# Kernel optimization log

Measured on AMD Instinct MI355X. Metric: run time of the kernel, lower is better.

The kernel has to match this reference:

```python
import jax, jax.numpy as jnp
import numpy as np

BANDWIDTH = 1.0  # init arg `bandwidth`
N, V, C = 8, 2048, 64


def setup_inputs() -> dict:
    key = jax.random.key(0)
    k1, k2 = jax.random.split(key)
    x = jax.random.normal(k1, (N, V, C), dtype=jnp.float32)
    # nn.Parameter(torch.rand(V, V)) -> uniform[0,1)
    weight = jax.random.uniform(k2, (V, V), dtype=jnp.float32)
    return {"x": x, "weight": weight}


def _pairwise_l2(x):
    # x: (N, V, C) -> dist[n,i,j] = ||x[n,i] - x[n,j]||_2, without the O(V^2*C) blow-up
    sq = jnp.sum(x * x, axis=-1)                                  # (N, V)
    d2 = sq[:, :, None] + sq[:, None, :] - 2.0 * jnp.einsum('nic,njc->nij', x, x)
    d2 = jnp.maximum(d2, 0.0)
    # safe sqrt: subgradient 0 at 0 (matches torch.norm), avoids NaN grads on the diagonal
    safe = jnp.where(d2 > 0, d2, 1.0)
    return jnp.where(d2 > 0, jnp.sqrt(safe), 0.0)


def reference(x, weight):
    dist = _pairwise_l2(x)                                        # (N, V, V)
    adj = jnp.exp((-0.5 / (BANDWIDTH ** 2)) * dist)               # Gaussian kernel on L2 (not squared)
    adj = jnp.einsum('nij,jk->nik', adj, weight)                  # (N, V, V) @ (V, V)
    return jax.nn.softmax(adj, axis=-1)
```

## Files before the change

kernel.cpp:

```cpp
#include <hip/hip_runtime.h>
#include <hip/hip_bf16.h>
#include <hip/hip_fp16.h>
#include <math.h>

#define V 2048
#define C 64
#define NB 8
#define M_TOTAL (NB * V)

typedef __attribute__((ext_vector_type(8))) short bf16x8;
typedef __attribute__((ext_vector_type(4))) float f32x4;

static __device__ __forceinline__ unsigned short f2bf(float f) {
    __hip_bfloat16 h = __float2bfloat16(f);
    return *reinterpret_cast<unsigned short*>(&h);
}
static __device__ __forceinline__ unsigned short f2h(float f) {
    __half h = __float2half(f);
    return *reinterpret_cast<unsigned short*>(&h);
}
static __device__ __forceinline__ float h2f(unsigned short u) {
    __half h = *reinterpret_cast<__half*>(&u);
    return __half2float(h);
}

#define GLOAD_LDS16(g, l)                                                        \
    __builtin_amdgcn_global_load_lds((const __attribute__((address_space(1))) void*)(g), \
                                     (__attribute__((address_space(3))) void*)(l), 16, 0, 0)


__global__ __launch_bounds__(256) void q_kernel(const float* __restrict__ x,
                                                float* __restrict__ q) {
    const int gw   = blockIdx.x * 4 + (threadIdx.x >> 6);
    const int lane = threadIdx.x & 63;
    const int lr = lane & 15, lq = lane >> 4;

    const float* rp = x + (size_t)(gw * 16 + lr) * C + lq * 8;
    float4 f0 = *(const float4*)(rp);
    float4 f1 = *(const float4*)(rp + 4);
    float4 f2 = *(const float4*)(rp + 32);
    float4 f3 = *(const float4*)(rp + 36);

    bf16x8 a0, a1;
    a0[0] = (short)f2bf(f0.x); a0[1] = (short)f2bf(f0.y);
    a0[2] = (short)f2bf(f0.z); a0[3] = (short)f2bf(f0.w);
    a0[4] = (short)f2bf(f1.x); a0[5] = (short)f2bf(f1.y);
    a0[6] = (short)f2bf(f1.z); a0[7] = (short)f2bf(f1.w);
    a1[0] = (short)f2bf(f2.x); a1[1] = (short)f2bf(f2.y);
    a1[2] = (short)f2bf(f2.z); a1[3] = (short)f2bf(f2.w);
    a1[4] = (short)f2bf(f3.x); a1[5] = (short)f2bf(f3.y);
    a1[6] = (short)f2bf(f3.z); a1[7] = (short)f2bf(f3.w);

    f32x4 acc = (f32x4){0.f, 0.f, 0.f, 0.f};
    acc = __builtin_amdgcn_mfma_f32_16x16x32_bf16(a0, a0, acc, 0, 0, 0);
    acc = __builtin_amdgcn_mfma_f32_16x16x32_bf16(a1, a1, acc, 0, 0, 0);

    const int r = lr;
    if (lq == (r >> 2)) q[gw * 16 + r] = acc[r & 3];
}

__global__ __launch_bounds__(256) void adj_mfma(const float* __restrict__ x,
                                                const float* __restrict__ q,
                                                unsigned short* __restrict__ adjb) {
    const int n  = blockIdx.z;
    const int i0 = blockIdx.y * 128;
    const int j0 = blockIdx.x * 128;
    const size_t nV = (size_t)n * V;

    __shared__ short Xi[128][72];
    __shared__ short Xj[128][72];
    __shared__ float Qi[128];
    __shared__ float Qj[128];

    const float* xn = x + nV * C;
    const int tid = threadIdx.x;

    for (int idx = tid; idx < 1024; idx += 256) {
        const int row = idx >> 3;
        const int c8  = (idx & 7) * 8;
        float4 ai0 = *(const float4*)(xn + (size_t)(i0 + row) * C + c8);
        float4 ai1 = *(const float4*)(xn + (size_t)(i0 + row) * C + c8 + 4);
        float4 aj0 = *(const float4*)(xn + (size_t)(j0 + row) * C + c8);
        float4 aj1 = *(const float4*)(xn + (size_t)(j0 + row) * C + c8 + 4);
        bf16x8 pi, pj;
        pi[0] = (short)f2bf(ai0.x); pi[1] = (short)f2bf(ai0.y);
        pi[2] = (short)f2bf(ai0.z); pi[3] = (short)f2bf(ai0.w);
        pi[4] = (short)f2bf(ai1.x); pi[5] = (short)f2bf(ai1.y);
        pi[6] = (short)f2bf(ai1.z); pi[7] = (short)f2bf(ai1.w);
        pj[0] = (short)f2bf(aj0.x); pj[1] = (short)f2bf(aj0.y);
        pj[2] = (short)f2bf(aj0.z); pj[3] = (short)f2bf(aj0.w);
        pj[4] = (short)f2bf(aj1.x); pj[5] = (short)f2bf(aj1.y);
        pj[6] = (short)f2bf(aj1.z); pj[7] = (short)f2bf(aj1.w);
        *(bf16x8*)&Xi[row][c8] = pi;
        *(bf16x8*)&Xj[row][c8] = pj;
    }
    if (tid < 128)       Qi[tid]        = q[nV + i0 + tid];
    else                 Qj[tid - 128]  = q[nV + j0 + (tid - 128)];
    __syncthreads();

    const int wid  = tid >> 6;
    const int lane = tid & 63;
    const int wr = wid >> 1, wc = wid & 1;
    const int lr = lane & 15, lq = lane >> 4;

    bf16x8 a[4][2], b[4][2];
#pragma unroll
    for (int m = 0; m < 4; ++m) {
        a[m][0] = *(const bf16x8*)&Xi[wr * 64 + m * 16 + lr][lq * 8];
        a[m][1] = *(const bf16x8*)&Xi[wr * 64 + m * 16 + lr][32 + lq * 8];
    }
#pragma unroll
    for (int nn = 0; nn < 4; ++nn) {
        b[nn][0] = *(const bf16x8*)&Xj[wc * 64 + nn * 16 + lr][lq * 8];
        b[nn][1] = *(const bf16x8*)&Xj[wc * 64 + nn * 16 + lr][32 + lq * 8];
    }

#pragma unroll
    for (int m = 0; m < 4; ++m) {
#pragma unroll
        for (int nn = 0; nn < 4; ++nn) {
            f32x4 g = (f32x4){0.f, 0.f, 0.f, 0.f};
            g = __builtin_amdgcn_mfma_f32_16x16x32_bf16(a[m][0], b[nn][0], g, 0, 0, 0);
            g = __builtin_amdgcn_mfma_f32_16x16x32_bf16(a[m][1], b[nn][1], g, 0, 0, 0);
            const int col_l = wc * 64 + nn * 16 + lr;
            const float qj = Qj[col_l];
#pragma unroll
            for (int r = 0; r < 4; ++r) {
                const int row_l = wr * 64 + m * 16 + lq * 4 + r;
                float d2 = Qi[row_l] + qj - 2.0f * g[r];
                d2 = fmaxf(d2, 0.0f);
                const float e = expf(-0.5f * sqrtf(d2));
                adjb[(nV + i0 + row_l) * V + j0 + col_l] = f2bf(e);
            }
        }
    }
}

__global__ __launch_bounds__(256) void wt_kernel(const float* __restrict__ w,
                                                 unsigned short* __restrict__ wt) {
    __shared__ float tile[64][65];
    const int r0 = blockIdx.y * 64, c0 = blockIdx.x * 64;
    const int tr = threadIdx.x >> 4;
    const int tc4 = (threadIdx.x & 15) << 2;
#pragma unroll
    for (int it = 0; it < 4; ++it) {
        const int r = tr + 16 * it;
        float4 v = *(const float4*)(w + (size_t)(r0 + r) * V + c0 + tc4);
        tile[r][tc4 + 0] = v.x; tile[r][tc4 + 1] = v.y;
        tile[r][tc4 + 2] = v.z; tile[r][tc4 + 3] = v.w;
    }
    __syncthreads();
#pragma unroll
    for (int it = 0; it < 4; ++it) {
        const int cr = tr + 16 * it;
        ushort4 o;
        o.x = f2bf(tile[tc4 + 0][cr]);
        o.y = f2bf(tile[tc4 + 1][cr]);
        o.z = f2bf(tile[tc4 + 2][cr]);
        o.w = f2bf(tile[tc4 + 3][cr]);
        *(ushort4*)(wt + (size_t)(c0 + cr) * V + r0 + tc4) = o;
    }
}

__device__ __forceinline__ void stage_region(char* smem, int regionOff,
                                             const unsigned short* gbase,
                                             int tile, int ks, int tid) {
#pragma unroll
    for (int s = 0; s < 2; ++s) {
        const int off = s * 8192 + tid * 16;
        const int row = off >> 6;
        const int pb  = off & 63;
        const int lb  = pb ^ (((row >> 1) & 3) << 4);
        const unsigned short* g = gbase + (size_t)row * V + tile * 64 + ks * 32 + (lb >> 1);
        GLOAD_LDS16(g, smem + regionOff + off);
    }
}

#define LDS_FRAG(BUF, BOFF, KS, ROW)                                             \
    (*(const bf16x8*)(smem + (BUF) * 65536 + (BOFF) + (KS) * 16384 +             \
                      (ROW) * 64 + (lqb ^ ((((ROW) >> 1) & 3) << 4))))

#define PHASE(BUF, MS, KS, LOADB, STAGE_STMT, WAITV)                             \
    {                                                                            \
        bf16x8 af[4];                                                            \
        _Pragma("unroll") for (int m = 0; m < 4; ++m) {                          \
            const int row = wr128 + ((MS) + m) * 16 + lr;                        \
            af[m] = LDS_FRAG(BUF, 0, KS, row);                                   \
        }                                                                        \
        if (LOADB) {                                                             \
            _Pragma("unroll") for (int n = 0; n < 4; ++n) {                      \
                const int row = wc64 + n * 16 + lr;                              \
                bf[n] = LDS_FRAG(BUF, 32768, KS, row);                           \
            }                                                                    \
        }                                                                        \
        STAGE_STMT;                                                              \
        if (WAITV) {                                                             \
            asm volatile("s_waitcnt vmcnt(6)" ::: "memory");                     \
            __builtin_amdgcn_sched_barrier(0);                                   \
        }                                                                        \
        __builtin_amdgcn_s_barrier();                                            \
        asm volatile("s_waitcnt lgkmcnt(0)" ::: "memory");                       \
        __builtin_amdgcn_sched_barrier(0);                                       \
        __builtin_amdgcn_s_setprio(1);                                           \
        _Pragma("unroll") for (int m = 0; m < 4; ++m)                            \
            _Pragma("unroll") for (int n = 0; n < 4; ++n)                        \
                acc[(MS) + m][n] = __builtin_amdgcn_mfma_f32_16x16x32_bf16(      \
                    af[m], bf[n], acc[(MS) + m][n], 0, 0, 0);                    \
        __builtin_amdgcn_s_setprio(0);                                           \
        __builtin_amdgcn_s_barrier();                                            \
    }

template <int FUSED>
__global__ __launch_bounds__(512, 2) void gemm_8ph(const unsigned short* __restrict__ adjb,
                                                   const unsigned short* __restrict__ wtb,
                                                   float* __restrict__ out,
                                                   unsigned short* __restrict__ expw,
                                                   float* __restrict__ partial) {
    extern __shared__ char smem[];

    const int bid = blockIdx.x;
    const int swz = (bid & 7) * 64 + (bid >> 3);
    const int by = swz >> 3;
    const int bx = swz & 7;
    const int i0 = by * 256;
    const int n0 = bx * 256;

    const int tid  = threadIdx.x;
    const int wid  = tid >> 6;
    const int lane = tid & 63;
    const int wr = wid >> 2, wc = wid & 3;
    const int wr128 = wr * 128, wc64 = wc * 64;
    const int lr = lane & 15, lq = lane >> 4;
    const int lqb = lq * 16;

    const unsigned short* gA = adjb + (size_t)i0 * V;
    const unsigned short* gB = wtb  + (size_t)n0 * V;

    f32x4 acc[8][4];
#pragma unroll
    for (int m = 0; m < 8; ++m)
#pragma unroll
        for (int n = 0; n < 4; ++n) acc[m][n] = (f32x4){0.f, 0.f, 0.f, 0.f};

    stage_region(smem, 32768,         gB, 0, 0, tid);
    stage_region(smem, 0,             gA, 0, 0, tid);
    stage_region(smem, 49152,         gB, 0, 1, tid);
    stage_region(smem, 16384,         gA, 0, 1, tid);
    stage_region(smem, 65536 + 32768, gB, 1, 0, tid);
    stage_region(smem, 65536 + 0,     gA, 1, 0, tid);
    stage_region(smem, 65536 + 49152, gB, 1, 1, tid);
    asm volatile("s_waitcnt vmcnt(6)" ::: "memory");
    __builtin_amdgcn_sched_barrier(0);
    __builtin_amdgcn_s_barrier();

    bf16x8 bf[4];

#pragma unroll 1
    for (int i = 0; i < 16; ++i) {
        const int t1b = 2 * i + 1;
        const int t2  = (2 * i + 2 < 32) ? 2 * i + 2 : 31;
        const int t3  = (2 * i + 3 < 32) ? 2 * i + 3 : 31;

        PHASE(0, 0, 0, true,  stage_region(smem, 65536 + 16384, gA, t1b, 1, tid), false)
        PHASE(0, 4, 0, false, stage_region(smem, 32768,         gB, t2,  0, tid), false)
        PHASE(0, 0, 1, true,  stage_region(smem, 0,             gA, t2,  0, tid), false)
        PHASE(0, 4, 1, false, stage_region(smem, 49152,         gB, t2,  1, tid), true)
        PHASE(1, 0, 0, true,  stage_region(smem, 16384,         gA, t2,  1, tid), false)
        PHASE(1, 4, 0, false, stage_region(smem, 65536 + 32768, gB, t3,  0, tid), false)
        PHASE(1, 0, 1, true,  stage_region(smem, 65536 + 0,     gA, t3,  0, tid), false)
        PHASE(1, 4, 1, false, stage_region(smem, 65536 + 49152, gB, t3,  1, tid), true)
    }

    if (FUSED) {
        unsigned short* ep = expw + (size_t)(i0 + wr128) * V + n0 + wc64;
        const int slot = bx * 4 + wc;
#pragma unroll
        for (int m = 0; m < 8; ++m) {
            float rp[4] = {0.f, 0.f, 0.f, 0.f};
#pragma unroll
            for (int n = 0; n < 4; ++n)
#pragma unroll
                for (int r = 0; r < 4; ++r) {
                    const float e = expf(acc[m][n][r]);
                    rp[r] += e;
                    ep[(size_t)(m * 16 + lq * 4 + r) * V + n * 16 + lr] = f2h(e);
                }
#pragma unroll
            for (int r = 0; r < 4; ++r) {
                rp[r] += __shfl_xor(rp[r], 1);
                rp[r] += __shfl_xor(rp[r], 2);
                rp[r] += __shfl_xor(rp[r], 4);
                rp[r] += __shfl_xor(rp[r], 8);
            }
            if (lr == 0) {
#pragma unroll
                for (int r = 0; r < 4; ++r)
                    partial[(size_t)(i0 + wr128 + m * 16 + lq * 4 + r) * 32 + slot] = rp[r];
            }
        }
    } else {
        float* op = out + (size_t)(i0 + wr128) * V + n0 + wc64;
#pragma unroll
        for (int m = 0; m < 8; ++m)
#pragma unroll
            for (int n = 0; n < 4; ++n)
#pragma unroll
                for (int r = 0; r < 4; ++r)
                    op[(size_t)(m * 16 + lq * 4 + r) * V + n * 16 + lr] = acc[m][n][r];
    }
}

__global__ __launch_bounds__(256) void normalize_kernel(const unsigned short* __restrict__ expw,
                                                        const float* __restrict__ partial,
                                                        float* __restrict__ out) {
    const int row  = blockIdx.x * 4 + (threadIdx.x >> 6);
    const int lane = threadIdx.x & 63;

    float s = (lane < 32) ? partial[(size_t)row * 32 + lane] : 0.0f;
#pragma unroll
    for (int o = 32; o; o >>= 1) s += __shfl_xor(s, o);
    const float inv = 1.0f / s;

    const unsigned short* ip = expw + (size_t)row * V;
    float* op = out + (size_t)row * V;
#pragma unroll
    for (int t = 0; t < 4; ++t) {
        const int base = (t * 64 + lane) * 8;
        ushort4 u0 = *(const ushort4*)(ip + base);
        ushort4 u1 = *(const ushort4*)(ip + base + 4);
        float4 o0, o1;
        o0.x = h2f(u0.x) * inv; o0.y = h2f(u0.y) * inv;
        o0.z = h2f(u0.z) * inv; o0.w = h2f(u0.w) * inv;
        o1.x = h2f(u1.x) * inv; o1.y = h2f(u1.y) * inv;
        o1.z = h2f(u1.z) * inv; o1.w = h2f(u1.w) * inv;
        *(float4*)(op + base)     = o0;
        *(float4*)(op + base + 4) = o1;
    }
}

__global__ __launch_bounds__(256) void gemm_mfma(const unsigned short* __restrict__ adjb,
                                                 const unsigned short* __restrict__ wtb,
                                                 float* __restrict__ out) {
    const int bid = blockIdx.x;
    const int swz = (bid & 7) * 256 + (bid >> 3);
    const int by = swz >> 4;
    const int bx = swz & 15;
    const int i0 = by * 128;
    const int n0 = bx * 128;

    __shared__ alignas(16) unsigned short As[128 * 32];
    __shared__ alignas(16) unsigned short Bs[128 * 32];

    const int tid  = threadIdx.x;
    const int wid  = tid >> 6;
    const int lane = tid & 63;
    const int wr = wid >> 1, wc = wid & 1;
    const int lr = lane & 15, lq = lane >> 4;

    f32x4 acc[4][4];
#pragma unroll
    for (int m = 0; m < 4; ++m)
#pragma unroll
        for (int n = 0; n < 4; ++n) acc[m][n] = (f32x4){0.f, 0.f, 0.f, 0.f};

    const unsigned short* ga = adjb + (size_t)(i0 + (tid >> 2)) * V + (tid & 3) * 8;
    const unsigned short* gb = wtb  + (size_t)(n0 + (tid >> 2)) * V + (tid & 3) * 8;
    unsigned short* lA = &As[tid * 8];
    unsigned short* lB = &Bs[tid * 8];
    const size_t rowskip = (size_t)64 * V;

    for (int kt = 0; kt < 64; ++kt) {
        const int k0 = kt * 32;
        if (kt) __syncthreads();
        GLOAD_LDS16(ga + k0,           lA);
        GLOAD_LDS16(ga + rowskip + k0, lA + 256 * 8);
        GLOAD_LDS16(gb + k0,           lB);
        GLOAD_LDS16(gb + rowskip + k0, lB + 256 * 8);
        __syncthreads();

        bf16x8 a[4], b[4];
#pragma unroll
        for (int m = 0; m < 4; ++m)
            a[m] = *(const bf16x8*)&As[(wr * 64 + m * 16 + lr) * 32 + lq * 8];
#pragma unroll
        for (int n = 0; n < 4; ++n)
            b[n] = *(const bf16x8*)&Bs[(wc * 64 + n * 16 + lr) * 32 + lq * 8];
#pragma unroll
        for (int m = 0; m < 4; ++m)
#pragma unroll
            for (int n = 0; n < 4; ++n)
                acc[m][n] = __builtin_amdgcn_mfma_f32_16x16x32_bf16(a[m], b[n], acc[m][n], 0, 0, 0);
    }

    float* outp = out + (size_t)(i0 + wr * 64) * V + n0 + wc * 64;
#pragma unroll
    for (int m = 0; m < 4; ++m) {
        const int r0 = m * 16 + lq * 4;
#pragma unroll
        for (int n = 0; n < 4; ++n) {
            const int cc = n * 16 + lr;
#pragma unroll
            for (int r = 0; r < 4; ++r)
                outp[(size_t)(r0 + r) * V + cc] = acc[m][n][r];
        }
    }
}


__global__ __launch_bounds__(256) void adj_kernel(const float* __restrict__ x,
                                                  float* __restrict__ adj) {
    const int n  = blockIdx.z;
    const int i0 = blockIdx.y * 64;
    const int j0 = blockIdx.x * 64;

    __shared__ float Xi[64][65];
    __shared__ float Xj[64][65];

    const float* xn = x + (size_t)n * V * C;
    const int tid = threadIdx.x;
    const int lr = tid >> 4;
    const int lc = (tid & 15) << 2;
#pragma unroll
    for (int it = 0; it < 4; ++it) {
        const int r = lr + it * 16;
        float4 vi = *(const float4*)(xn + (size_t)(i0 + r) * C + lc);
        float4 vj = *(const float4*)(xn + (size_t)(j0 + r) * C + lc);
        Xi[r][lc + 0] = vi.x; Xi[r][lc + 1] = vi.y; Xi[r][lc + 2] = vi.z; Xi[r][lc + 3] = vi.w;
        Xj[r][lc + 0] = vj.x; Xj[r][lc + 1] = vj.y; Xj[r][lc + 2] = vj.z; Xj[r][lc + 3] = vj.w;
    }
    __syncthreads();

    const int ti = (tid >> 4) << 2;
    const int tj = (tid & 15) << 2;

    float acc[4][4] = {};
#pragma unroll 4
    for (int c = 0; c < C; ++c) {
        float ai[4], bj[4];
#pragma unroll
        for (int a = 0; a < 4; ++a) ai[a] = Xi[ti + a][c];
#pragma unroll
        for (int b = 0; b < 4; ++b) bj[b] = Xj[tj + b][c];
#pragma unroll
        for (int a = 0; a < 4; ++a)
#pragma unroll
            for (int b = 0; b < 4; ++b) {
                const float d = ai[a] - bj[b];
                acc[a][b] = fmaf(d, d, acc[a][b]);
            }
    }

    float* outb = adj + ((size_t)n * V + i0) * V + j0;
#pragma unroll
    for (int a = 0; a < 4; ++a) {
        float4 o0;
        o0.x = expf(-0.5f * sqrtf(acc[a][0]));
        o0.y = expf(-0.5f * sqrtf(acc[a][1]));
        o0.z = expf(-0.5f * sqrtf(acc[a][2]));
        o0.w = expf(-0.5f * sqrtf(acc[a][3]));
        *(float4*)(outb + (size_t)(ti + a) * V + tj) = o0;
    }
}

__global__ __launch_bounds__(256) void gemm_inplace(float* __restrict__ adjout,
                                                    const float* __restrict__ w) {
    const int n  = blockIdx.y;
    const int i0 = blockIdx.x * 8;

    __shared__ float rows[8][V];

    float* base = adjout + ((size_t)n * V + i0) * V;
    const int tid = threadIdx.x;

    for (int t = tid; t < (8 * V) / 4; t += 256) {
        const int r = t >> 9;
        const int c = (t & 511) << 2;
        float4 v = *(const float4*)(base + (size_t)r * V + c);
        rows[r][c + 0] = v.x; rows[r][c + 1] = v.y; rows[r][c + 2] = v.z; rows[r][c + 3] = v.w;
    }
    __syncthreads();

    float acc[8][8] = {};
    const int k0 = tid << 3;
    const float* wp = w + k0;

    for (int j = 0; j < V; ++j) {
        float a[8];
#pragma unroll
        for (int r = 0; r < 8; ++r) a[r] = rows[r][j];
        const float* wr = wp + (size_t)j * V;
        const float4 w0 = *(const float4*)(wr);
        const float4 w1 = *(const float4*)(wr + 4);
        const float wv[8] = {w0.x, w0.y, w0.z, w0.w, w1.x, w1.y, w1.z, w1.w};
#pragma unroll
        for (int r = 0; r < 8; ++r)
#pragma unroll
            for (int c = 0; c < 8; ++c)
                acc[r][c] = fmaf(a[r], wv[c], acc[r][c]);
    }

#pragma unroll
    for (int r = 0; r < 8; ++r) {
        float4 o0, o1;
        o0.x = acc[r][0]; o0.y = acc[r][1]; o0.z = acc[r][2]; o0.w = acc[r][3];
        o1.x = acc[r][4]; o1.y = acc[r][5]; o1.z = acc[r][6]; o1.w = acc[r][7];
        *(float4*)(base + (size_t)r * V + k0)     = o0;
        *(float4*)(base + (size_t)r * V + k0 + 4) = o1;
    }
}

__global__ __launch_bounds__(256) void softmax_kernel(float* __restrict__ out) {
    const int row  = blockIdx.x * 4 + (threadIdx.x >> 6);
    const int lane = threadIdx.x & 63;
    float* p = out + (size_t)row * V;

    float4 v[8];
#pragma unroll
    for (int s = 0; s < 8; ++s)
        v[s] = *(const float4*)(p + (size_t)(s * 64 + lane) * 4);

    float m = -INFINITY;
#pragma unroll
    for (int s = 0; s < 8; ++s)
        m = fmaxf(m, fmaxf(fmaxf(v[s].x, v[s].y), fmaxf(v[s].z, v[s].w)));
#pragma unroll
    for (int o = 32; o; o >>= 1) m = fmaxf(m, __shfl_xor(m, o));

    float sum = 0.0f;
#pragma unroll
    for (int s = 0; s < 8; ++s) {
        v[s].x = expf(v[s].x - m);
        v[s].y = expf(v[s].y - m);
        v[s].z = expf(v[s].z - m);
        v[s].w = expf(v[s].w - m);
        sum += (v[s].x + v[s].y) + (v[s].z + v[s].w);
    }
#pragma unroll
    for (int o = 32; o; o >>= 1) sum += __shfl_xor(sum, o);

    const float inv = 1.0f / sum;
#pragma unroll
    for (int s = 0; s < 8; ++s) {
        float4 o4;
        o4.x = v[s].x * inv; o4.y = v[s].y * inv;
        o4.z = v[s].z * inv; o4.w = v[s].w * inv;
        *(float4*)(p + (size_t)(s * 64 + lane) * 4) = o4;
    }
}

extern "C" void kernel_launch(void* const* d_in, const int* in_sizes, int n_in,
                              void* d_out, int out_size, void* d_ws, size_t ws_size,
                              hipStream_t stream) {
    const float* x = (const float*)d_in[0];
    const float* w = (const float*)d_in[1];
    float* out = (float*)d_out;

    const size_t adj_elems = (size_t)M_TOTAL * V;
    const size_t wt_elems  = (size_t)V * V;
    const size_t need      = (adj_elems + wt_elems) * 2;
    const size_t exp_off   = need;
    const size_t part_off  = exp_off + adj_elems * 2;
    const size_t need_big  = part_off + (size_t)M_TOTAL * 32 * 4;

    if (ws_size >= need) {
        unsigned short* adjb = (unsigned short*)d_ws;
        unsigned short* wtb  = adjb + adj_elems;
        float* q = out;

        q_kernel<<<M_TOTAL / 64, 256, 0, stream>>>(x, q);
        adj_mfma<<<dim3(V / 128, V / 128, NB), 256, 0, stream>>>(x, q, adjb);
        wt_kernel<<<dim3(V / 64, V / 64), 256, 0, stream>>>(w, wtb);

        if (ws_size >= need_big) {
            unsigned short* expw = (unsigned short*)((char*)d_ws + exp_off);
            float* partial       = (float*)((char*)d_ws + part_off);
            hipError_t ok = hipFuncSetAttribute(
                reinterpret_cast<const void*>(&gemm_8ph<1>),
                hipFuncAttributeMaxDynamicSharedMemorySize, 131072);
            if (ok == hipSuccess) {
                gemm_8ph<1><<<512, 512, 131072, stream>>>(adjb, wtb, out, expw, partial);
                normalize_kernel<<<M_TOTAL / 4, 256, 0, stream>>>(expw, partial, out);
                return;
            }
        }
        hipError_t ok = hipFuncSetAttribute(
            reinterpret_cast<const void*>(&gemm_8ph<0>),
            hipFuncAttributeMaxDynamicSharedMemorySize, 131072);
        if (ok == hipSuccess) {
            gemm_8ph<0><<<512, 512, 131072, stream>>>(adjb, wtb, out, nullptr, nullptr);
        } else {
            gemm_mfma<<<2048, 256, 0, stream>>>(adjb, wtb, out);
        }
        softmax_kernel<<<(NB * V) / 4, 256, 0, stream>>>(out);
    } else {
        dim3 g1(V / 64, V / 64, NB);
        adj_kernel<<<g1, 256, 0, stream>>>(x, out);
        dim3 g2(V / 8, NB);
        gemm_inplace<<<g2, 256, 0, stream>>>(out, w);
        softmax_kernel<<<(NB * V) / 4, 256, 0, stream>>>(out);
    }
}
```

Baseline: 211.4 us.

## Fuse row-norm computation into adj kernel and move softmax sums to normalize

```diff
diff --git a/kernel.cpp b/kernel.cpp
--- a/kernel.cpp
+++ b/kernel.cpp
@@ -29,38 +29,7 @@
                                      (__attribute__((address_space(3))) void*)(l), 16, 0, 0)
 
 
-__global__ __launch_bounds__(256) void q_kernel(const float* __restrict__ x,
-                                                float* __restrict__ q) {
-    const int gw   = blockIdx.x * 4 + (threadIdx.x >> 6);
-    const int lane = threadIdx.x & 63;
-    const int lr = lane & 15, lq = lane >> 4;
-
-    const float* rp = x + (size_t)(gw * 16 + lr) * C + lq * 8;
-    float4 f0 = *(const float4*)(rp);
-    float4 f1 = *(const float4*)(rp + 4);
-    float4 f2 = *(const float4*)(rp + 32);
-    float4 f3 = *(const float4*)(rp + 36);
-
-    bf16x8 a0, a1;
-    a0[0] = (short)f2bf(f0.x); a0[1] = (short)f2bf(f0.y);
-    a0[2] = (short)f2bf(f0.z); a0[3] = (short)f2bf(f0.w);
-    a0[4] = (short)f2bf(f1.x); a0[5] = (short)f2bf(f1.y);
-    a0[6] = (short)f2bf(f1.z); a0[7] = (short)f2bf(f1.w);
-    a1[0] = (short)f2bf(f2.x); a1[1] = (short)f2bf(f2.y);
-    a1[2] = (short)f2bf(f2.z); a1[3] = (short)f2bf(f2.w);
-    a1[4] = (short)f2bf(f3.x); a1[5] = (short)f2bf(f3.y);
-    a1[6] = (short)f2bf(f3.z); a1[7] = (short)f2bf(f3.w);
-
-    f32x4 acc = (f32x4){0.f, 0.f, 0.f, 0.f};
-    acc = __builtin_amdgcn_mfma_f32_16x16x32_bf16(a0, a0, acc, 0, 0, 0);
-    acc = __builtin_amdgcn_mfma_f32_16x16x32_bf16(a1, a1, acc, 0, 0, 0);
-
-    const int r = lr;
-    if (lq == (r >> 2)) q[gw * 16 + r] = acc[r & 3];
-}
-
 __global__ __launch_bounds__(256) void adj_mfma(const float* __restrict__ x,
-                                                const float* __restrict__ q,
                                                 unsigned short* __restrict__ adjb) {
     const int n  = blockIdx.z;
     const int i0 = blockIdx.y * 128;
@@ -94,14 +63,36 @@
         *(bf16x8*)&Xi[row][c8] = pi;
         *(bf16x8*)&Xj[row][c8] = pj;
     }
-    if (tid < 128)       Qi[tid]        = q[nV + i0 + tid];
-    else                 Qj[tid - 128]  = q[nV + j0 + (tid - 128)];
     __syncthreads();
 
     const int wid  = tid >> 6;
     const int lane = tid & 63;
     const int wr = wid >> 1, wc = wid & 1;
     const int lr = lane & 15, lq = lane >> 4;
+
+#pragma unroll
+    for (int gg = 0; gg < 2; ++gg) {
+        const int g = wid * 2 + gg;
+        {
+            const short* xr = &Xi[g * 16 + lr][0];
+            bf16x8 a0 = *(const bf16x8*)(xr + lq * 8);
+            bf16x8 a1 = *(const bf16x8*)(xr + 32 + lq * 8);
+            f32x4 qa = (f32x4){0.f, 0.f, 0.f, 0.f};
+            qa = __builtin_amdgcn_mfma_f32_16x16x32_bf16(a0, a0, qa, 0, 0, 0);
+            qa = __builtin_amdgcn_mfma_f32_16x16x32_bf16(a1, a1, qa, 0, 0, 0);
+            if (lq == (lr >> 2)) Qi[g * 16 + lr] = qa[lr & 3];
+        }
+        {
+            const short* xr = &Xj[g * 16 + lr][0];
+            bf16x8 a0 = *(const bf16x8*)(xr + lq * 8);
+            bf16x8 a1 = *(const bf16x8*)(xr + 32 + lq * 8);
+            f32x4 qa = (f32x4){0.f, 0.f, 0.f, 0.f};
+            qa = __builtin_amdgcn_mfma_f32_16x16x32_bf16(a0, a0, qa, 0, 0, 0);
+            qa = __builtin_amdgcn_mfma_f32_16x16x32_bf16(a1, a1, qa, 0, 0, 0);
+            if (lq == (lr >> 2)) Qj[g * 16 + lr] = qa[lr & 3];
+        }
+    }
+    __syncthreads();
 
     bf16x8 a[4][2], b[4][2];
 #pragma unroll
@@ -129,7 +120,7 @@
                 const int row_l = wr * 64 + m * 16 + lq * 4 + r;
                 float d2 = Qi[row_l] + qj - 2.0f * g[r];
                 d2 = fmaxf(d2, 0.0f);
-                const float e = expf(-0.5f * sqrtf(d2));
+                const float e = __expf(-0.5f * sqrtf(d2));
                 adjb[(nV + i0 + row_l) * V + j0 + col_l] = f2bf(e);
             }
         }
@@ -214,8 +205,7 @@
 __global__ __launch_bounds__(512, 2) void gemm_8ph(const unsigned short* __restrict__ adjb,
                                                    const unsigned short* __restrict__ wtb,
                                                    float* __restrict__ out,
-                                                   unsigned short* __restrict__ expw,
-                                                   float* __restrict__ partial) {
+                                                   unsigned short* __restrict__ expw) {
     extern __shared__ char smem[];
 
     const int bid = blockIdx.x;
@@ -273,29 +263,14 @@
 
     if (FUSED) {
         unsigned short* ep = expw + (size_t)(i0 + wr128) * V + n0 + wc64;
-        const int slot = bx * 4 + wc;
 #pragma unroll
         for (int m = 0; m < 8; ++m) {
-            float rp[4] = {0.f, 0.f, 0.f, 0.f};
-#pragma unroll
-            for (int n = 0; n < 4; ++n)
-#pragma unroll
-                for (int r = 0; r < 4; ++r) {
-                    const float e = expf(acc[m][n][r]);
-                    rp[r] += e;
-                    ep[(size_t)(m * 16 + lq * 4 + r) * V + n * 16 + lr] = f2h(e);
-                }
 #pragma unroll
             for (int r = 0; r < 4; ++r) {
-                rp[r] += __shfl_xor(rp[r], 1);
-                rp[r] += __shfl_xor(rp[r], 2);
-                rp[r] += __shfl_xor(rp[r], 4);
-                rp[r] += __shfl_xor(rp[r], 8);
-            }
-            if (lr == 0) {
-#pragma unroll
-                for (int r = 0; r < 4; ++r)
-                    partial[(size_t)(i0 + wr128 + m * 16 + lq * 4 + r) * 32 + slot] = rp[r];
+                unsigned short* p = ep + (size_t)(m * 16 + lq * 4 + r) * V;
+#pragma unroll
+                for (int n = 0; n < 4; ++n)
+                    p[n * 16 + lr] = f2h(__expf(acc[m][n][r]));
             }
         }
     } else {
@@ -311,28 +286,39 @@
 }
 
 __global__ __launch_bounds__(256) void normalize_kernel(const unsigned short* __restrict__ expw,
-                                                        const float* __restrict__ partial,
                                                         float* __restrict__ out) {
     const int row  = blockIdx.x * 4 + (threadIdx.x >> 6);
     const int lane = threadIdx.x & 63;
 
-    float s = (lane < 32) ? partial[(size_t)row * 32 + lane] : 0.0f;
-#pragma unroll
-    for (int o = 32; o; o >>= 1) s += __shfl_xor(s, o);
-    const float inv = 1.0f / s;
-
     const unsigned short* ip = expw + (size_t)row * V;
     float* op = out + (size_t)row * V;
+
+    float v[32];
+    float sum = 0.0f;
 #pragma unroll
     for (int t = 0; t < 4; ++t) {
         const int base = (t * 64 + lane) * 8;
         ushort4 u0 = *(const ushort4*)(ip + base);
         ushort4 u1 = *(const ushort4*)(ip + base + 4);
+        v[t * 8 + 0] = h2f(u0.x); v[t * 8 + 1] = h2f(u0.y);
+        v[t * 8 + 2] = h2f(u0.z); v[t * 8 + 3] = h2f(u0.w);
+        v[t * 8 + 4] = h2f(u1.x); v[t * 8 + 5] = h2f(u1.y);
+        v[t * 8 + 6] = h2f(u1.z); v[t * 8 + 7] = h2f(u1.w);
+#pragma unroll
+        for (int k = 0; k < 8; ++k) sum += v[t * 8 + k];
+    }
+#pragma unroll
+    for (int o = 32; o; o >>= 1) sum += __shfl_xor(sum, o);
+    const float inv = 1.0f / sum;
+
+#pragma unroll
+    for (int t = 0; t < 4; ++t) {
+        const int base = (t * 64 + lane) * 8;
         float4 o0, o1;
-        o0.x = h2f(u0.x) * inv; o0.y = h2f(u0.y) * inv;
-        o0.z = h2f(u0.z) * inv; o0.w = h2f(u0.w) * inv;
-        o1.x = h2f(u1.x) * inv; o1.y = h2f(u1.y) * inv;
-        o1.z = h2f(u1.z) * inv; o1.w = h2f(u1.w) * inv;
+        o0.x = v[t * 8 + 0] * inv; o0.y = v[t * 8 + 1] * inv;
+        o0.z = v[t * 8 + 2] * inv; o0.w = v[t * 8 + 3] * inv;
+        o1.x = v[t * 8 + 4] * inv; o1.y = v[t * 8 + 5] * inv;
+        o1.z = v[t * 8 + 6] * inv; o1.w = v[t * 8 + 7] * inv;
         *(float4*)(op + base)     = o0;
         *(float4*)(op + base + 4) = o1;
     }
@@ -559,27 +545,23 @@
     const size_t wt_elems  = (size_t)V * V;
     const size_t need      = (adj_elems + wt_elems) * 2;
     const size_t exp_off   = need;
-    const size_t part_off  = exp_off + adj_elems * 2;
-    const size_t need_big  = part_off + (size_t)M_TOTAL * 32 * 4;
+    const size_t need_big  = exp_off + adj_elems * 2;
 
     if (ws_size >= need) {
         unsigned short* adjb = (unsigned short*)d_ws;
         unsigned short* wtb  = adjb + adj_elems;
-        float* q = out;
-
-        q_kernel<<<M_TOTAL / 64, 256, 0, stream>>>(x, q);
-        adj_mfma<<<dim3(V / 128, V / 128, NB), 256, 0, stream>>>(x, q, adjb);
+
+        adj_mfma<<<dim3(V / 128, V / 128, NB), 256, 0, stream>>>(x, adjb);
         wt_kernel<<<dim3(V / 64, V / 64), 256, 0, stream>>>(w, wtb);
 
         if (ws_size >= need_big) {
             unsigned short* expw = (unsigned short*)((char*)d_ws + exp_off);
-            float* partial       = (float*)((char*)d_ws + part_off);
             hipError_t ok = hipFuncSetAttribute(
                 reinterpret_cast<const void*>(&gemm_8ph<1>),
                 hipFuncAttributeMaxDynamicSharedMemorySize, 131072);
             if (ok == hipSuccess) {
-                gemm_8ph<1><<<512, 512, 131072, stream>>>(adjb, wtb, out, expw, partial);
-                normalize_kernel<<<M_TOTAL / 4, 256, 0, stream>>>(expw, partial, out);
+                gemm_8ph<1><<<512, 512, 131072, stream>>>(adjb, wtb, out, expw);
+                normalize_kernel<<<M_TOTAL / 4, 256, 0, stream>>>(expw, out);
                 return;
             }
         }
@@ -587,7 +569,7 @@
             reinterpret_cast<const void*>(&gemm_8ph<0>),
             hipFuncAttributeMaxDynamicSharedMemorySize, 131072);
         if (ok == hipSuccess) {
-            gemm_8ph<0><<<512, 512, 131072, stream>>>(adjb, wtb, out, nullptr, nullptr);
+            gemm_8ph<0><<<512, 512, 131072, stream>>>(adjb, wtb, out, nullptr);
         } else {
             gemm_mfma<<<2048, 256, 0, stream>>>(adjb, wtb, out);
         }
```

After: 188.8 us, median of 2. 10.7% less time.
